# Performance work log

Hardware: AMD Instinct MI355X
Metric: run time of the kernel (lower is better)

## Reference

```python
import jax, jax.numpy as jnp
import numpy as np

TOKEN_DIM = 256
N_HEADS = 8
HEAD_DIM = TOKEN_DIM // N_HEADS


def setup_inputs() -> dict:
    key = jax.random.key(0)
    ks = jax.random.split(key, 10)
    B, S, D = 4, 2048, TOKEN_DIM
    s = 1.0 / np.sqrt(D)
    return {
        "x": jax.random.normal(ks[0], (B, S, D), dtype=jnp.float32),
        "Wq": jax.random.uniform(ks[1], (D, D), jnp.float32, -s, s),
        "bq": jax.random.uniform(ks[2], (D,), jnp.float32, -s, s),
        "Wk": jax.random.uniform(ks[3], (D, D), jnp.float32, -s, s),
        "bk": jax.random.uniform(ks[4], (D,), jnp.float32, -s, s),
        "Wv": jax.random.uniform(ks[5], (D, D), jnp.float32, -s, s),
        "bv": jax.random.uniform(ks[6], (D,), jnp.float32, -s, s),
        "Wo": jax.random.uniform(ks[7], (D, D), jnp.float32, -s, s),
        "bo": jax.random.uniform(ks[8], (D,), jnp.float32, -s, s),
        "head_scale": jnp.ones((N_HEADS,), dtype=jnp.float32),
    }


def reference(x, Wq, bq, Wk, bk, Wv, bv, Wo, bo, head_scale):
    B, S, D = x.shape
    H, Hd = N_HEADS, HEAD_DIM
    scale = jnp.asarray(np.sqrt(Hd), x.dtype)

    def split_heads(t):
        return t.reshape(B, S, H, Hd).transpose(0, 2, 1, 3)  # (B,H,S,Hd)

    Q = split_heads(x @ Wq.T + bq)
    K = split_heads(x @ Wk.T + bk)
    V = split_heads(x @ Wv.T + bv)

    scores = jnp.einsum("bhsd,bhtd->bhst", Q, K) / scale  # (B,H,S,S)
    attn = jax.nn.softmax(scores, axis=-1)
    attn_scaled = attn * head_scale[None, :, None, None]
    Hctx = jnp.einsum("bhst,bhtd->bhsd", attn_scaled, V)
    Hctx = Hctx.transpose(0, 2, 1, 3).reshape(B, S, D)
    return Hctx @ Wo.T + bo
```

## Files before the change

### kernel.cpp

```cpp
#include <hip/hip_runtime.h>
#include <hip/hip_bf16.h>
#include <math.h>

#define B_ 4
#define S_ 2048
#define D_ 256
#define H_ 8
#define HD_ 32

typedef __attribute__((ext_vector_type(8))) short short8;
typedef __attribute__((ext_vector_type(4))) short short4v;
typedef __attribute__((ext_vector_type(4))) float floatx4;
typedef unsigned short ushort_t;
typedef unsigned int uint_t;

typedef union { unsigned u[2]; short4v v4; } PkU;

#define CVT_PK(DST, LO, HI) \
  asm volatile("v_cvt_pk_bf16_f32 %0, %1, %2" : "=v"(DST) : "v"(LO), "v"(HI))

#define MFMA16(ACC, A, B) \
  asm volatile("v_mfma_f32_16x16x16_bf16 %0, %1, %2, %0" : "+v"(ACC) : "v"(A), "v"(B))

__device__ __forceinline__ ushort_t f2bf(float f) {
  union { float f; unsigned u; } v; v.f = f;
  unsigned u = v.u;
  unsigned r = (u + 0x7FFFu + ((u >> 16) & 1u)) >> 16;
  return (ushort_t)r;
}

__global__ __launch_bounds__(256)
void cvt_all(const float* __restrict__ x,
             const float* __restrict__ wq, const float* __restrict__ wk,
             const float* __restrict__ wv, const float* __restrict__ wo,
             ushort_t* __restrict__ xb,
             ushort_t* __restrict__ wqb, ushort_t* __restrict__ wkb,
             ushort_t* __restrict__ wvb, ushort_t* __restrict__ wob)
{
  const int b = blockIdx.x;
  const float4* s; uint2* d; int i;
  if (b < 2048) {
    s = (const float4*)x; d = (uint2*)xb; i = b * 256 + threadIdx.x;
  } else {
    int r = b - 2048; int mm = r >> 6;
    s = (const float4*)(mm == 0 ? wq : mm == 1 ? wk : mm == 2 ? wv : wo);
    d = (uint2*)(mm == 0 ? wqb : mm == 1 ? wkb : mm == 2 ? wvb : wob);
    i = (r & 63) * 256 + threadIdx.x;
  }
  float4 f = s[i];
  uint2 o;
  CVT_PK(o.x, f.x, f.y);
  CVT_PK(o.y, f.z, f.w);
  d[i] = o;
}

__global__ __launch_bounds__(256)
void proj_qkv(const ushort_t* __restrict__ xb,
              const ushort_t* __restrict__ wq, const ushort_t* __restrict__ wk, const ushort_t* __restrict__ wv,
              const float* __restrict__ bq, const float* __restrict__ bk, const float* __restrict__ bv,
              ushort_t* __restrict__ qout, ushort_t* __restrict__ kout, ushort_t* __restrict__ vout)
{
  __shared__ __align__(16) ushort_t W_lds[64 * 264];

  const int z = blockIdx.z;
  const ushort_t* wb = (z == 0) ? wq : (z == 1) ? wk : wv;
  const float* bias  = (z == 0) ? bq : (z == 1) ? bk : bv;

  const int t = threadIdx.x;
  const int l = t & 63;
  const int w = t >> 6;
  const int row0 = blockIdx.y * 128 + w * 16;
  const int col0 = blockIdx.x * 64;
  const int lr = l & 15, lg = l >> 4, lk = lg * 8;

  {
    const ushort_t* wsrc = wb + (col0 + (t >> 2)) * D_ + (t & 3) * 64;
    ushort_t* wdst = &W_lds[(t >> 2) * 264 + (t & 3) * 64];
#pragma unroll
    for (int i = 0; i < 8; ++i)
      *(uint4*)(wdst + i * 8) = *(const uint4*)(wsrc + i * 8);
  }
  __syncthreads();

  floatx4 acc[2][4] = {};
  const ushort_t* arow0 = xb + (row0 + lr) * D_ + lk;
  const ushort_t* arow1 = xb + (row0 + 64 + lr) * D_ + lk;
#pragma unroll
  for (int kk = 0; kk < D_; kk += 32) {
    short8 a0 = *(const short8*)(arow0 + kk);
    short8 a1 = *(const short8*)(arow1 + kk);
#pragma unroll
    for (int j = 0; j < 4; ++j) {
      short8 b = *(const short8*)&W_lds[(j * 16 + lr) * 264 + kk + lk];
      acc[0][j] = __builtin_amdgcn_mfma_f32_16x16x32_bf16(a0, b, acc[0][j], 0, 0, 0);
      acc[1][j] = __builtin_amdgcn_mfma_f32_16x16x32_bf16(a1, b, acc[1][j], 0, 0, 0);
    }
  }

  if (z == 2) {
#pragma unroll
    for (int rs = 0; rs < 2; ++rs)
#pragma unroll
      for (int j = 0; j < 4; ++j) {
        int c = col0 + j * 16 + lr;
        float bv_ = bias[c];
        int hh = c >> 5, d = c & 31;
        int i0 = row0 + rs * 64 + lg * 4;
        int bb = i0 >> 11, s0 = i0 & 2047;
        uint2 pv;
        CVT_PK(pv.x, acc[rs][j][0] + bv_, acc[rs][j][1] + bv_);
        CVT_PK(pv.y, acc[rs][j][2] + bv_, acc[rs][j][3] + bv_);
        *(uint2*)&vout[(((size_t)(bb * H_ + hh)) * HD_ + d) * S_ + s0] = pv;
      }
  } else {
    ushort_t* dst = (z == 0) ? qout : kout;
    const float qscale = (z == 0) ? 0.25503486f : 1.0f;
#pragma unroll
    for (int rs = 0; rs < 2; ++rs)
#pragma unroll
      for (int j = 0; j < 4; ++j) {
        int c = col0 + j * 16 + lr;
        float bv_ = bias[c];
        int hh = c >> 5, d = c & 31;
#pragma unroll
        for (int rp = 0; rp < 2; ++rp) {
          int i = row0 + rs * 64 + lg * 4 + rp * 2;
          int bb = i >> 11, s = i & 2047;
          uint_t pr;
          CVT_PK(pr, (acc[rs][j][rp*2] + bv_) * qscale, (acc[rs][j][rp*2+1] + bv_) * qscale);
          size_t b0 = ((size_t)(bb * H_ + hh) * S_ + s) * HD_ + d;
          dst[b0]       = (ushort_t)(pr & 0xffffu);
          dst[b0 + HD_] = (ushort_t)(pr >> 16);
        }
      }
  }
}

__global__ __launch_bounds__(256)
void attn_kernel(const ushort_t* __restrict__ qb, const ushort_t* __restrict__ kb,
                 const ushort_t* __restrict__ vtb, const float* __restrict__ head_scale,
                 ushort_t* __restrict__ hb)
{
  __shared__ __align__(16) ushort_t K_lds[2][128 * 40];
  __shared__ __align__(16) ushort_t Vt_lds[2][32 * 136];

  const int tid = threadIdx.x;
  const int l = tid & 63;
  const int w = tid >> 6;
  const int bh = blockIdx.y;
  const int qt = blockIdx.x;
  const int lr = l & 15;
  const int lg = l >> 4;

  const ushort_t* qp  = qb  + (size_t)bh * S_ * HD_;
  const ushort_t* kp  = kb  + (size_t)bh * S_ * HD_;
  const ushort_t* vtp = vtb + (size_t)bh * S_ * HD_;

  const int q0 = qt * 64 + w * 16;
  short8 qfrag = *(const short8*)(qp + (q0 + lr) * HD_ + lg * 8);

  floatx4 oA = {}, oB = {}, oL = {};

  const int kr = tid >> 1, kc = (tid & 1) * 16;
  const int vr = tid >> 3, vc = (tid & 7) * 16;

  const short4v ones4 = {0x3F80, 0x3F80, 0x3F80, 0x3F80};
  const floatx4 zero4 = {0.f, 0.f, 0.f, 0.f};

  uint4 kr0 = *(const uint4*)(kp + kr * HD_ + kc);
  uint4 kr1 = *(const uint4*)(kp + kr * HD_ + kc + 8);
  uint4 vr0 = *(const uint4*)(vtp + vr * S_ + vc);
  uint4 vr1 = *(const uint4*)(vtp + vr * S_ + vc + 8);
  *(uint4*)&K_lds[0][kr * 40 + kc]      = kr0;
  *(uint4*)&K_lds[0][kr * 40 + kc + 8]  = kr1;
  *(uint4*)&Vt_lds[0][vr * 136 + vc]     = vr0;
  *(uint4*)&Vt_lds[0][vr * 136 + vc + 8] = vr1;

  int cur = 0;
  for (int t0 = 0; t0 < S_; t0 += 128) {
    __syncthreads();

    const int tn = (t0 + 128) & (S_ - 1);
    kr0 = *(const uint4*)(kp + (tn + kr) * HD_ + kc);
    kr1 = *(const uint4*)(kp + (tn + kr) * HD_ + kc + 8);
    vr0 = *(const uint4*)(vtp + vr * S_ + tn + vc);
    vr1 = *(const uint4*)(vtp + vr * S_ + tn + vc + 8);

    floatx4 sv[8];
#pragma unroll
    for (int s = 0; s < 8; ++s) {
      short8 kf = *(const short8*)&K_lds[cur][(s * 16 + lr) * 40 + lg * 8];
      sv[s] = __builtin_amdgcn_mfma_f32_16x16x32_bf16(kf, qfrag, zero4, 0, 0, 0);
    }

#pragma unroll
    for (int s = 0; s < 8; ++s)
#pragma unroll
      for (int r = 0; r < 4; ++r)
        sv[s][r] = __builtin_amdgcn_exp2f(sv[s][r]);

    PkU pk[8];
#pragma unroll
    for (int s = 0; s < 8; ++s) {
      CVT_PK(pk[s].u[0], sv[s][0], sv[s][1]);
      CVT_PK(pk[s].u[1], sv[s][2], sv[s][3]);
    }

#pragma unroll
    for (int s = 0; s < 8; ++s) {
      const int cb = s * 16 + lg * 4;
      short4v a0 = *(const short4v*)&Vt_lds[cur][lr * 136 + cb];
      short4v a1 = *(const short4v*)&Vt_lds[cur][(16 + lr) * 136 + cb];
      MFMA16(oA, a0, pk[s].v4);
      MFMA16(oB, a1, pk[s].v4);
      MFMA16(oL, ones4, pk[s].v4);
    }

    *(uint4*)&K_lds[cur ^ 1][kr * 40 + kc]      = kr0;
    *(uint4*)&K_lds[cur ^ 1][kr * 40 + kc + 8]  = kr1;
    *(uint4*)&Vt_lds[cur ^ 1][vr * 136 + vc]     = vr0;
    *(uint4*)&Vt_lds[cur ^ 1][vr * 136 + vc + 8] = vr1;
    cur ^= 1;
  }

  asm volatile("s_nop 7\n\ts_nop 7" :::);
  const int bb = bh >> 3, hh = bh & 7;
  float inv = head_scale[hh] / oL[0];
  const int sq = q0 + lr;
  size_t base = ((size_t)(bb * S_ + sq)) * D_ + hh * HD_;
  uint2 w0, w1;
  CVT_PK(w0.x, oA[0] * inv, oA[1] * inv);
  CVT_PK(w0.y, oA[2] * inv, oA[3] * inv);
  CVT_PK(w1.x, oB[0] * inv, oB[1] * inv);
  CVT_PK(w1.y, oB[2] * inv, oB[3] * inv);
  *(uint2*)&hb[base + lg * 4] = w0;
  *(uint2*)&hb[base + 16 + lg * 4] = w1;
}

__global__ __launch_bounds__(256)
void proj_out(const ushort_t* __restrict__ hbm, const ushort_t* __restrict__ wo,
              const float* __restrict__ bo, float* __restrict__ out)
{
  __shared__ __align__(16) ushort_t W_lds[64 * 264];

  const int t = threadIdx.x;
  const int l = t & 63;
  const int w = t >> 6;
  const int row0 = blockIdx.y * 64 + w * 16;
  const int col0 = blockIdx.x * 64;
  const int lr = l & 15, lg = l >> 4, lk = lg * 8;

  {
    const ushort_t* wsrc = wo + (col0 + (t >> 2)) * D_ + (t & 3) * 64;
    ushort_t* wdst = &W_lds[(t >> 2) * 264 + (t & 3) * 64];
#pragma unroll
    for (int i = 0; i < 8; ++i)
      *(uint4*)(wdst + i * 8) = *(const uint4*)(wsrc + i * 8);
  }
  __syncthreads();

  floatx4 acc[4] = {};
  const ushort_t* arow = hbm + (row0 + lr) * D_ + lk;
#pragma unroll
  for (int kk = 0; kk < D_; kk += 32) {
    short8 a = *(const short8*)(arow + kk);
#pragma unroll
    for (int j = 0; j < 4; ++j) {
      short8 b = *(const short8*)&W_lds[(j * 16 + lr) * 264 + kk + lk];
      acc[j] = __builtin_amdgcn_mfma_f32_16x16x32_bf16(a, b, acc[j], 0, 0, 0);
    }
  }
#pragma unroll
  for (int j = 0; j < 4; ++j) {
    int c = col0 + j * 16 + lr;
    float bias = bo[c];
#pragma unroll
    for (int r = 0; r < 4; ++r) {
      int i = row0 + lg * 4 + r;
      out[(size_t)i * D_ + c] = acc[j][r] + bias;
    }
  }
}

extern "C" void kernel_launch(void* const* d_in, const int* in_sizes, int n_in,
                              void* d_out, int out_size, void* d_ws, size_t ws_size,
                              hipStream_t stream) {
  (void)in_sizes; (void)n_in; (void)out_size; (void)ws_size;
  const float* x  = (const float*)d_in[0];
  const float* Wq = (const float*)d_in[1];
  const float* bq = (const float*)d_in[2];
  const float* Wk = (const float*)d_in[3];
  const float* bk = (const float*)d_in[4];
  const float* Wv = (const float*)d_in[5];
  const float* bv = (const float*)d_in[6];
  const float* Wo = (const float*)d_in[7];
  const float* bo = (const float*)d_in[8];
  const float* hs = (const float*)d_in[9];

  char* ws = (char*)d_ws;
  ushort_t* xb  = (ushort_t*)ws;
  ushort_t* wqb = (ushort_t*)(ws + 4 * 1024 * 1024);
  ushort_t* wkb = wqb + 65536;
  ushort_t* wvb = wkb + 65536;
  ushort_t* wob = wvb + 65536;
  ushort_t* qb  = wob + 65536;
  ushort_t* kbb = qb + 2097152;
  ushort_t* vbb = kbb + 2097152;
  ushort_t* hbb = xb;

  cvt_all<<<2304, 256, 0, stream>>>(x, Wq, Wk, Wv, Wo, xb, wqb, wkb, wvb, wob);
  proj_qkv<<<dim3(4, 64, 3), 256, 0, stream>>>(xb, wqb, wkb, wvb, bq, bk, bv, qb, kbb, vbb);
  attn_kernel<<<dim3(32, 32), 256, 0, stream>>>(qb, kbb, vbb, hs, hbb);
  proj_out<<<dim3(4, 128), 256, 0, stream>>>(hbb, wob, bo, (float*)d_out);
}
```

Before: 63.06 us.

## Pad V LDS rows, swizzle block-to-head mapping, use builtin PV MFMA with priority

The V^T LDS row stride changes from 136 to 140 elements, which avoids bank conflicts on the 8-byte PV operand reads; the stores are split into 8-byte writes to match the new alignment. The flat block index is remapped so consecutive blocks cover different (batch, head) pairs, changing L2 locality. The inline-asm PV MFMA is replaced by the compiler builtin when available, so the compiler can schedule it, and the PV loop runs at raised wave priority through s_setprio. The cost is more LDS store instructions and a mapping that assumes a 32x32 grid.

After: 63.99 us. About the same (+1.5%).

```diff
diff --git a/kernel.cpp b/kernel.cpp
--- a/kernel.cpp
+++ b/kernel.cpp
@@ -19,8 +19,13 @@
 #define CVT_PK(DST, LO, HI) \
   asm volatile("v_cvt_pk_bf16_f32 %0, %1, %2" : "=v"(DST) : "v"(LO), "v"(HI))
 
-#define MFMA16(ACC, A, B) \
+#if __has_builtin(__builtin_amdgcn_mfma_f32_16x16x16bf16_1k)
+#define PV_MFMA(ACC, A, B) \
+  ACC = __builtin_amdgcn_mfma_f32_16x16x16bf16_1k(A, B, ACC, 0, 0, 0)
+#else
+#define PV_MFMA(ACC, A, B) \
   asm volatile("v_mfma_f32_16x16x16_bf16 %0, %1, %2, %0" : "+v"(ACC) : "v"(A), "v"(B))
+#endif
 
 __device__ __forceinline__ ushort_t f2bf(float f) {
   union { float f; unsigned u; } v; v.f = f;
@@ -142,13 +147,14 @@
                  ushort_t* __restrict__ hb)
 {
   __shared__ __align__(16) ushort_t K_lds[2][128 * 40];
-  __shared__ __align__(16) ushort_t Vt_lds[2][32 * 136];
+  __shared__ __align__(16) ushort_t Vt_lds[2][32 * 140];
 
   const int tid = threadIdx.x;
   const int l = tid & 63;
   const int w = tid >> 6;
-  const int bh = blockIdx.y;
-  const int qt = blockIdx.x;
+  const int f = blockIdx.y * 32 + blockIdx.x;
+  const int qt = f >> 5;
+  const int bh = (f & 7) * 4 + ((f >> 3) & 3);
   const int lr = l & 15;
   const int lg = l >> 4;
 
@@ -169,12 +175,17 @@
 
   uint4 kr0 = *(const uint4*)(kp + kr * HD_ + kc);
   uint4 kr1 = *(const uint4*)(kp + kr * HD_ + kc + 8);
-  uint4 vr0 = *(const uint4*)(vtp + vr * S_ + vc);
-  uint4 vr1 = *(const uint4*)(vtp + vr * S_ + vc + 8);
-  *(uint4*)&K_lds[0][kr * 40 + kc]      = kr0;
-  *(uint4*)&K_lds[0][kr * 40 + kc + 8]  = kr1;
-  *(uint4*)&Vt_lds[0][vr * 136 + vc]     = vr0;
-  *(uint4*)&Vt_lds[0][vr * 136 + vc + 8] = vr1;
+  uint4 vv0 = *(const uint4*)(vtp + vr * S_ + vc);
+  uint4 vv1 = *(const uint4*)(vtp + vr * S_ + vc + 8);
+  *(uint4*)&K_lds[0][kr * 40 + kc]     = kr0;
+  *(uint4*)&K_lds[0][kr * 40 + kc + 8] = kr1;
+  {
+    ushort_t* vd = &Vt_lds[0][vr * 140 + vc];
+    *(uint2*)(vd)      = make_uint2(vv0.x, vv0.y);
+    *(uint2*)(vd + 4)  = make_uint2(vv0.z, vv0.w);
+    *(uint2*)(vd + 8)  = make_uint2(vv1.x, vv1.y);
+    *(uint2*)(vd + 12) = make_uint2(vv1.z, vv1.w);
+  }
 
   int cur = 0;
   for (int t0 = 0; t0 < S_; t0 += 128) {
@@ -183,8 +194,8 @@
     const int tn = (t0 + 128) & (S_ - 1);
     kr0 = *(const uint4*)(kp + (tn + kr) * HD_ + kc);
     kr1 = *(const uint4*)(kp + (tn + kr) * HD_ + kc + 8);
-    vr0 = *(const uint4*)(vtp + vr * S_ + tn + vc);
-    vr1 = *(const uint4*)(vtp + vr * S_ + tn + vc + 8);
+    vv0 = *(const uint4*)(vtp + vr * S_ + tn + vc);
+    vv1 = *(const uint4*)(vtp + vr * S_ + tn + vc + 8);
 
     floatx4 sv[8];
 #pragma unroll
@@ -206,20 +217,27 @@
       CVT_PK(pk[s].u[1], sv[s][2], sv[s][3]);
     }
 
+    __builtin_amdgcn_s_setprio(1);
 #pragma unroll
     for (int s = 0; s < 8; ++s) {
       const int cb = s * 16 + lg * 4;
-      short4v a0 = *(const short4v*)&Vt_lds[cur][lr * 136 + cb];
-      short4v a1 = *(const short4v*)&Vt_lds[cur][(16 + lr) * 136 + cb];
-      MFMA16(oA, a0, pk[s].v4);
-      MFMA16(oB, a1, pk[s].v4);
-      MFMA16(oL, ones4, pk[s].v4);
-    }
-
-    *(uint4*)&K_lds[cur ^ 1][kr * 40 + kc]      = kr0;
-    *(uint4*)&K_lds[cur ^ 1][kr * 40 + kc + 8]  = kr1;
-    *(uint4*)&Vt_lds[cur ^ 1][vr * 136 + vc]     = vr0;
-    *(uint4*)&Vt_lds[cur ^ 1][vr * 136 + vc + 8] = vr1;
+      short4v a0 = *(const short4v*)&Vt_lds[cur][lr * 140 + cb];
+      short4v a1 = *(const short4v*)&Vt_lds[cur][(16 + lr) * 140 + cb];
+      PV_MFMA(oA, a0, pk[s].v4);
+      PV_MFMA(oB, a1, pk[s].v4);
+      PV_MFMA(oL, ones4, pk[s].v4);
+    }
+    __builtin_amdgcn_s_setprio(0);
+
+    *(uint4*)&K_lds[cur ^ 1][kr * 40 + kc]     = kr0;
+    *(uint4*)&K_lds[cur ^ 1][kr * 40 + kc + 8] = kr1;
+    {
+      ushort_t* vd = &Vt_lds[cur ^ 1][vr * 140 + vc];
+      *(uint2*)(vd)      = make_uint2(vv0.x, vv0.y);
+      *(uint2*)(vd + 4)  = make_uint2(vv0.z, vv0.w);
+      *(uint2*)(vd + 8)  = make_uint2(vv1.x, vv1.y);
+      *(uint2*)(vd + 12) = make_uint2(vv1.z, vv1.w);
+    }
     cur ^= 1;
   }
 
```
